# Performance work log

Hardware: AMD Instinct MI355X
Metric: run time of the kernel (lower is better)

Reference implementation:

```python
import jax, jax.numpy as jnp
import numpy as np

B, S, HID = 2, 2048, 2048
H = 16
HD = HID // H            # 128
HD2 = HD // 2            # 64 (rope dim per head)
LAT = HID // 8           # 256 latent dim
BASE = 10000.0


def _rotary_table(seq_len):
    # inv_freq over rope dim HD2
    inv_freq = 1.0 / (BASE ** (jnp.arange(0, HD2, 2, dtype=jnp.float32) / HD2))  # [HD2//2]
    pos = jnp.arange(seq_len, dtype=jnp.float32)
    sincos = pos[:, None] * inv_freq[None, :]                 # [S, HD2//2]
    return jnp.concatenate([jnp.sin(sincos), jnp.cos(sincos)], axis=-1)  # [S, HD2]


def _apply_rope(x, emb):
    # x: [B, S, H, HD2]; emb: [S, HD2]
    half = HD2 // 2
    x1, x2 = x[..., :half], x[..., half:]
    sin = emb[None, :, None, :half]
    cos = emb[None, :, None, half:]
    return jnp.concatenate([x1 * cos - x2 * sin, x1 * sin + x2 * cos], axis=-1)


def setup_inputs() -> dict:
    key = jax.random.key(0)
    ks = jax.random.split(key, 9)
    s = 0.02
    return {
        "hidden_states": jax.random.normal(ks[0], (B, S, HID), jnp.float32),
        "w_kv_d": jax.random.normal(ks[1], (HID, LAT), jnp.float32) * s,
        "w_q_d": jax.random.normal(ks[2], (HID, LAT), jnp.float32) * s,
        "w_k_u": jax.random.normal(ks[3], (LAT, H * HD2), jnp.float32) * s,
        "w_q_u": jax.random.normal(ks[4], (LAT, H * HD2), jnp.float32) * s,
        "w_v_u": jax.random.normal(ks[5], (LAT, H * HD), jnp.float32) * s,
        "w_rope_k": jax.random.normal(ks[6], (HID, HID // 2), jnp.float32) * s,
        "w_rope_q": jax.random.normal(ks[7], (LAT, HID // 2), jnp.float32) * s,
        "w_o": jax.random.normal(ks[8], (HID, HID), jnp.float32) * s,
    }


def reference(hidden_states, w_kv_d, w_q_d, w_k_u, w_q_u, w_v_u, w_rope_k, w_rope_q, w_o):
    b, s, _ = hidden_states.shape
    kv_d = hidden_states @ w_kv_d            # [B,S,LAT]
    q_d = hidden_states @ w_q_d              # [B,S,LAT]
    k_p = (kv_d @ w_k_u).reshape(b, s, H, HD2)
    q_p = (q_d @ w_q_u).reshape(b, s, H, HD2)
    v = (kv_d @ w_v_u).reshape(b, s, H, HD)
    k_r = (hidden_states @ w_rope_k).reshape(b, s, H, HD2)
    q_r = (q_d @ w_rope_q).reshape(b, s, H, HD2)

    emb = _rotary_table(s)
    k_r = _apply_rope(k_r, emb)
    q_r = _apply_rope(q_r, emb)

    k = jnp.concatenate([k_p, k_r], axis=-1)  # [B,S,H,HD]
    q = jnp.concatenate([q_p, q_r], axis=-1)

    scores = jnp.einsum('bqhd,bkhd->bhqk', q, k) / jnp.sqrt(jnp.float32(HD))
    causal = jnp.tril(jnp.ones((s, s), dtype=bool))
    scores = jnp.where(causal[None, None], scores, jnp.float32(-1e9))
    probs = jax.nn.softmax(scores, axis=-1)
    out = jnp.einsum('bhqk,bkhd->bqhd', probs, v).reshape(b, s, HID)
    return out @ w_o
```

## Files before the change

kernel.cpp:

```cpp
#include <hip/hip_runtime.h>
#include <hip/hip_bf16.h>

#define BB 2
#define SS 2048
#define HID 2048
#define NH 16
#define BS (BB*SS)
#define SCALE 0.088388347648318447f
#define C2LOG 0.12751743f

typedef __bf16 bf16x8 __attribute__((ext_vector_type(8)));
typedef float f32x4 __attribute__((ext_vector_type(4)));
typedef float f32x16 __attribute__((ext_vector_type(16)));
typedef unsigned int uintx2 __attribute__((ext_vector_type(2)));

__device__ __forceinline__ bf16x8 ld_frag(const __hip_bfloat16* p) {
    uint4 u = *reinterpret_cast<const uint4*>(p);
    return __builtin_bit_cast(bf16x8, u);
}
__device__ __forceinline__ void store_c(__hip_bfloat16* C, size_t idx, float v) {
    C[idx] = __float2bfloat16(v);
}
__device__ __forceinline__ void store_c(float* C, size_t idx, float v) {
    C[idx] = v;
}
__device__ __forceinline__ ushort bf_bits(float v) {
    __hip_bfloat16 h = __float2bfloat16(v);
    return *reinterpret_cast<ushort*>(&h);
}

#define GLD16(gp, lp) \
  __builtin_amdgcn_global_load_lds((const __attribute__((address_space(1))) void*)(gp), \
                                   (__attribute__((address_space(3))) void*)(lp), 16, 0, 0)

__global__ __launch_bounds__(256) void convert_kernel(
    const float* __restrict__ src, __hip_bfloat16* __restrict__ dst, int n8)
{
    int i = blockIdx.x * blockDim.x + threadIdx.x;
    if (i >= n8) return;
    float4 a = reinterpret_cast<const float4*>(src)[2 * i];
    float4 b = reinterpret_cast<const float4*>(src)[2 * i + 1];
    ushort u[8] = { bf_bits(a.x), bf_bits(a.y), bf_bits(a.z), bf_bits(a.w),
                    bf_bits(b.x), bf_bits(b.y), bf_bits(b.z), bf_bits(b.w) };
    reinterpret_cast<uint4*>(dst)[i] = *reinterpret_cast<uint4*>(u);
}

__global__ __launch_bounds__(256) void transpose_weights_kernel(
    const float* s0, const float* s1, const float* s2, const float* s3,
    const float* s4, const float* s5, const float* s6, const float* s7,
    __hip_bfloat16* WT1, __hip_bfloat16* WT2, __hip_bfloat16* WT3,
    __hip_bfloat16* WTo)
{
    const float* srcs[8] = { s0, s1, s2, s3, s4, s5, s6, s7 };
    const int Rs[8] = { 2048, 2048, 2048, 256, 256, 256, 256, 2048 };
    const int Cs[8] = { 256, 256, 1024, 1024, 2048, 1024, 1024, 2048 };
    __hip_bfloat16* dsts[8] = {
        WT1, WT1 + (size_t)256 * 2048, WT1 + (size_t)512 * 2048,
        WT2, WT2 + (size_t)1024 * 256,
        WT3, WT3 + (size_t)1024 * 256,
        WTo };
    const int prefix[9] = { 0, 512, 1024, 3072, 3328, 3840, 4096, 4352, 8448 };

    int bid = blockIdx.x;
    int seg = 0;
    #pragma unroll
    for (int i = 0; i < 8; i++) if (bid >= prefix[i + 1]) seg = i + 1;
    int local = bid - prefix[seg];
    int R = Rs[seg], C = Cs[seg];
    int tilesC = C / 32;
    int tr = local / tilesC, tc = local % tilesC;
    int r0 = tr * 32, c0 = tc * 32;
    const float* src = srcs[seg];
    __hip_bfloat16* dst = dsts[seg];

    __shared__ float Ts[32][33];
    int t = threadIdx.x;
    int ty = t >> 5, tx = t & 31;
    #pragma unroll
    for (int k = 0; k < 4; k++) {
        int r = ty + k * 8;
        Ts[r][tx] = src[(size_t)(r0 + r) * C + c0 + tx];
    }
    __syncthreads();
    #pragma unroll
    for (int k = 0; k < 4; k++) {
        int r = ty + k * 8;
        dst[(size_t)(c0 + r) * R + r0 + tx] = __float2bfloat16(Ts[tx][r]);
    }
}

template <typename TC>
__global__ __launch_bounds__(256) void gemm_bt_kernel(
    const __hip_bfloat16* __restrict__ A, int lda,
    const __hip_bfloat16* __restrict__ Bt,
    TC* __restrict__ C0, int ldc0, int sp0, int off0, float cm0,
    TC* __restrict__ C1, int ldc1, int sp1, int off1, float cm1,
    int splitN, int K)
{
    __shared__ alignas(16) __hip_bfloat16 As[128 * 32];
    __shared__ alignas(16) __hip_bfloat16 Bs[128 * 32];

    const int bn = blockIdx.x * 128;
    const int bm = blockIdx.y * 128;
    const int t = threadIdx.x;
    const int w = t >> 6;
    const int lane = t & 63;
    const int l15 = lane & 15;
    const int quad = lane >> 4;
    const int wm = (w & 1) * 64;
    const int wn = (w >> 1) * 64;

    const int srow = lane >> 2;
    const int skcol = (lane & 3) * 8;

    f32x4 acc[4][4] = {};

    for (int k0 = 0; k0 < K; k0 += 32) {
        __syncthreads();
        #pragma unroll
        for (int i = 0; i < 2; i++) {
            int r = w * 32 + i * 16 + srow;
            GLD16(A + (size_t)(bm + r) * lda + k0 + skcol, &As[r * 32 + skcol]);
            GLD16(Bt + (size_t)(bn + r) * K + k0 + skcol, &Bs[r * 32 + skcol]);
        }
        __syncthreads();

        bf16x8 af[4], bf[4];
        #pragma unroll
        for (int mt = 0; mt < 4; mt++)
            af[mt] = ld_frag(&As[(wm + mt * 16 + l15) * 32 + quad * 8]);
        #pragma unroll
        for (int nt = 0; nt < 4; nt++)
            bf[nt] = ld_frag(&Bs[(wn + nt * 16 + l15) * 32 + quad * 8]);
        #pragma unroll
        for (int mt = 0; mt < 4; mt++)
            #pragma unroll
            for (int nt = 0; nt < 4; nt++)
                acc[mt][nt] = __builtin_amdgcn_mfma_f32_16x16x32_bf16(
                    af[mt], bf[nt], acc[mt][nt], 0, 0, 0);
    }

    #pragma unroll
    for (int nt = 0; nt < 4; nt++) {
        int col = bn + wn + nt * 16 + l15;
        TC* Cp; int c, ld, s64, off; float cm;
        if (col < splitN) { Cp = C0; c = col; ld = ldc0; s64 = sp0; off = off0; cm = cm0; }
        else { Cp = C1; c = col - splitN; ld = ldc1; s64 = sp1; off = off1; cm = cm1; }
        if (s64 == 2) {
            #pragma unroll
            for (int mt = 0; mt < 4; mt++) {
                int row0 = bm + wm + mt * 16 + quad * 4;
                #pragma unroll
                for (int r = 0; r < 4; r++)
                    store_c(Cp, (size_t)c * 4096 + row0 + r, acc[mt][nt][r] * cm);
            }
        } else {
            int oc = s64 ? ((c >> 6) * 128 + (c & 63) + off) : c;
            #pragma unroll
            for (int mt = 0; mt < 4; mt++) {
                #pragma unroll
                for (int r = 0; r < 4; r++) {
                    int row = bm + wm + mt * 16 + quad * 4 + r;
                    store_c(Cp, (size_t)row * ld + oc, acc[mt][nt][r] * cm);
                }
            }
        }
    }
}

__global__ __launch_bounds__(256) void rope_kernel(
    __hip_bfloat16* __restrict__ Kb, __hip_bfloat16* __restrict__ Qb)
{
    int idx = blockIdx.x * blockDim.x + threadIdx.x;
    if (idx >= BS * NH * 32) return;
    int i = idx & 31;
    int h = (idx >> 5) & 15;
    int row = idx >> 9;
    int s = row & (SS - 1);

    float inv = exp2f(-(float)i * 0.4152410118609203f);
    float ang = (float)s * inv;
    float sn = sinf(ang), cs = cosf(ang);

    size_t obase = (size_t)row * 2048 + h * 128 + 64 + i;
    {
        float x1 = __bfloat162float(Kb[obase]);
        float x2 = __bfloat162float(Kb[obase + 32]);
        Kb[obase]      = __float2bfloat16(x1 * cs - x2 * sn);
        Kb[obase + 32] = __float2bfloat16(x1 * sn + x2 * cs);
    }
    {
        float x1 = __bfloat162float(Qb[obase]);
        float x2 = __bfloat162float(Qb[obase + 32]);
        Qb[obase]      = __float2bfloat16(x1 * cs - x2 * sn);
        Qb[obase + 32] = __float2bfloat16(x1 * sn + x2 * cs);
    }
}

__global__ __launch_bounds__(512) void flash_attn_kernel(
    const __hip_bfloat16* __restrict__ Q,
    const __hip_bfloat16* __restrict__ Kb,
    const __hip_bfloat16* __restrict__ Vt,
    __hip_bfloat16* __restrict__ O)
{
    __shared__ alignas(16) __hip_bfloat16 Ktd[2 * 4 * 64 * 32];
    __shared__ alignas(16) __hip_bfloat16 Vs[2 * 128 * 32];

    const int p = blockIdx.x;
    const int h = blockIdx.y;
    const int b = blockIdx.z;
    const int t = threadIdx.x;
    const int w = t >> 6;
    const int lane = t & 63;
    const int l31 = lane & 31;
    const int hi = lane >> 5;
    const int swl = (l31 >> 1) & 3;

    const int qt = (w < 4) ? (15 - p) : p;
    const int wq = w & 3;
    const int q = qt * 128 + wq * 32 + l31;
    const int my_nt = 2 * qt + 2;
    const int nbig = 2 * (15 - p) + 2;

    const __hip_bfloat16* Kbase = Kb + (size_t)(b * SS) * 2048 + h * 128;
    const __hip_bfloat16* Vtb = Vt + (size_t)(h * 128) * 4096 + b * SS;

    bf16x8 qf[8];
    {
        const __hip_bfloat16* qrow = Q + (size_t)(b * SS + q) * 2048 + h * 128;
        #pragma unroll
        for (int s = 0; s < 8; s++)
            qf[s] = ld_frag(qrow + s * 16 + hi * 8);
    }

    const int Lr = lane >> 2;
    const int Lc = (lane & 3) ^ ((lane >> 3) & 3);

    float m_i = -INFINITY;
    float l_i = 0.0f;
    f32x16 acc[4] = {};

    const int kds = w >> 1, khalf = w & 1;
    const int vkvh = w >> 2, vdq = w & 3;

    #pragma unroll
    for (int i = 0; i < 2; i++)
        GLD16(Kbase + (size_t)(khalf * 32 + i * 16 + Lr) * 2048 + kds * 32 + Lc * 8,
              &Ktd[kds * 2048 + khalf * 1024 + i * 512 + lane * 8]);
    asm volatile("" :: "v"(qf[0]), "v"(qf[1]), "v"(qf[2]), "v"(qf[3]),
                       "v"(qf[4]), "v"(qf[5]), "v"(qf[6]), "v"(qf[7]));

    for (int kt = 0; kt < nbig; kt++) {
        const int kvb = kt * 64;
        const int par = kt & 1;
        const bool active = (kt < my_nt);

        __builtin_amdgcn_s_barrier();
        asm volatile("" ::: "memory");

        #pragma unroll
        for (int i = 0; i < 2; i++)
            GLD16(Vtb + (size_t)(vdq * 32 + i * 16 + Lr) * 4096
                      + kvb + vkvh * 32 + Lc * 8,
                  &Vs[vkvh * 4096 + vdq * 1024 + i * 512 + lane * 8]);
        {
            const int kvb1 = ((kt + 1 < nbig) ? kt + 1 : nbig - 1) * 64;
            __hip_bfloat16* kdst = &Ktd[((kt + 1) & 1) * 8192 + kds * 2048 + khalf * 1024];
            #pragma unroll
            for (int i = 0; i < 2; i++)
                GLD16(Kbase + (size_t)(kvb1 + khalf * 32 + i * 16 + Lr) * 2048
                          + kds * 32 + Lc * 8,
                      kdst + i * 512 + lane * 8);
        }
        asm volatile("s_waitcnt vmcnt(4)" ::: "memory");
        __builtin_amdgcn_s_barrier();
        asm volatile("" ::: "memory");

        uint4 af[4];
        if (active) {
            const __hip_bfloat16* kb_base = &Ktd[par * 8192];
            f32x16 st[2] = {};
            #pragma unroll
            for (int s = 0; s < 8; s++)
                #pragma unroll
                for (int kb = 0; kb < 2; kb++) {
                    bf16x8 kf = ld_frag(kb_base + (s >> 1) * 2048 + (kb * 32 + l31) * 32
                                        + ((2 * (s & 1) + hi) ^ swl) * 8);
                    st[kb] = __builtin_amdgcn_mfma_f32_32x32x16_bf16(
                        kf, qf[s], st[kb], 0, 0, 0);
                }

            const int thr = q - kvb - 4 * hi;
            float tmx = -INFINITY;
            #pragma unroll
            for (int kb = 0; kb < 2; kb++)
                #pragma unroll
                for (int g = 0; g < 4; g++)
                    #pragma unroll
                    for (int r = 0; r < 4; r++) {
                        const int e = g * 4 + r;
                        float v = (kb * 32 + 8 * g + r <= thr) ? st[kb][e] : -INFINITY;
                        st[kb][e] = v;
                        tmx = fmaxf(tmx, v);
                    }
            tmx = fmaxf(tmx, __shfl_xor(tmx, 32));
            const float m2x = tmx * C2LOG;

            const bool nosc = __all(m2x <= m_i + 8.0f);
            const float mnew = nosc ? m_i : fmaxf(m_i, m2x);
            float rs = 0.0f;
            #pragma unroll
            for (int kb = 0; kb < 2; kb++)
                #pragma unroll
                for (int e = 0; e < 16; e++) {
                    float pv = exp2f(fmaf(st[kb][e], C2LOG, -mnew));
                    st[kb][e] = pv;
                    rs += pv;
                }
            rs += __shfl_xor(rs, 32);
            if (!nosc) {
                const float alpha = exp2f(m_i - mnew);
                m_i = mnew;
                l_i *= alpha;
                #pragma unroll
                for (int dt = 0; dt < 4; dt++)
                    #pragma unroll
                    for (int e = 0; e < 16; e++)
                        acc[dt][e] *= alpha;
            }
            l_i += rs;

            #pragma unroll
            for (int kb = 0; kb < 2; kb++) {
                unsigned int pk[4][2];
                #pragma unroll
                for (int g = 0; g < 4; g++)
                    #pragma unroll
                    for (int i = 0; i < 2; i++) {
                        float2 fp = make_float2(st[kb][g * 4 + 2 * i],
                                                st[kb][g * 4 + 2 * i + 1]);
                        __hip_bfloat162 h2 = __float22bfloat162_rn(fp);
                        pk[g][i] = *reinterpret_cast<unsigned int*>(&h2);
                    }
                #pragma unroll
                for (int sl = 0; sl < 2; sl++) {
                    uintx2 r0 = __builtin_amdgcn_permlane32_swap(
                        pk[2 * sl][0], pk[2 * sl + 1][0], false, false);
                    uintx2 r1 = __builtin_amdgcn_permlane32_swap(
                        pk[2 * sl][1], pk[2 * sl + 1][1], false, false);
                    af[kb * 2 + sl] = make_uint4(r0[0], r1[0], r0[1], r1[1]);
                }
            }
        }

        asm volatile("s_waitcnt vmcnt(2)" ::: "memory");
        __builtin_amdgcn_s_barrier();
        asm volatile("" ::: "memory");

        if (active) {
            #pragma unroll
            for (int s = 0; s < 4; s++) {
                bf16x8 pf = __builtin_bit_cast(bf16x8, af[s]);
                #pragma unroll
                for (int dt = 0; dt < 4; dt++) {
                    bf16x8 vf = ld_frag(&Vs[(s >> 1) * 4096 + (dt * 32 + l31) * 32
                                            + ((2 * (s & 1) + hi) ^ swl) * 8]);
                    acc[dt] = __builtin_amdgcn_mfma_f32_32x32x16_bf16(
                        vf, pf, acc[dt], 0, 0, 0);
                }
            }
        }
    }

    const float inv_l = 1.0f / l_i;
    __hip_bfloat16* orow = O + (size_t)(b * SS + q) * 2048 + h * 128;
    #pragma unroll
    for (int dt = 0; dt < 4; dt++)
        #pragma unroll
        for (int g = 0; g < 4; g++) {
            ushort u[4];
            #pragma unroll
            for (int r = 0; r < 4; r++)
                u[r] = bf_bits(acc[dt][g * 4 + r] * inv_l);
            *reinterpret_cast<uint2*>(orow + dt * 32 + 8 * g + 4 * hi) =
                *reinterpret_cast<uint2*>(u);
        }
}

extern "C" void kernel_launch(void* const* d_in, const int* in_sizes, int n_in,
                              void* d_out, int out_size, void* d_ws, size_t ws_size,
                              hipStream_t stream)
{
    const float* hs       = (const float*)d_in[0];
    const float* w_kv_d   = (const float*)d_in[1];
    const float* w_q_d    = (const float*)d_in[2];
    const float* w_k_u    = (const float*)d_in[3];
    const float* w_q_u    = (const float*)d_in[4];
    const float* w_v_u    = (const float*)d_in[5];
    const float* w_rope_k = (const float*)d_in[6];
    const float* w_rope_q = (const float*)d_in[7];
    const float* w_o      = (const float*)d_in[8];
    float* out = (float*)d_out;

    char* p = (char*)d_ws;
    auto alloc = [&](size_t nelem) {
        __hip_bfloat16* r = (__hip_bfloat16*)p;
        p += nelem * sizeof(__hip_bfloat16);
        return r;
    };
    __hip_bfloat16* hsb  = alloc((size_t)BS * HID);
    __hip_bfloat16* qkvd = alloc((size_t)BS * 512);
    __hip_bfloat16* WT1  = alloc((size_t)1536 * 2048);
    __hip_bfloat16* WT2  = alloc((size_t)3072 * 256);
    __hip_bfloat16* WT3  = alloc((size_t)2048 * 256);
    __hip_bfloat16* WTo  = alloc((size_t)2048 * 2048);
    __hip_bfloat16* Kbuf = alloc((size_t)BS * HID);
    __hip_bfloat16* Qbuf = alloc((size_t)BS * HID);
    __hip_bfloat16* Vtb  = alloc((size_t)HID * BS);
    __hip_bfloat16* attn = hsb;

    dim3 blk(256);

    convert_kernel<<<dim3((BS * HID / 8 + 255) / 256), blk, 0, stream>>>(
        hs, hsb, BS * HID / 8);
    transpose_weights_kernel<<<dim3(8448), blk, 0, stream>>>(
        w_kv_d, w_q_d, w_rope_k, w_k_u, w_v_u, w_q_u, w_rope_q, w_o,
        WT1, WT2, WT3, WTo);

    gemm_bt_kernel<__hip_bfloat16><<<dim3(1536 / 128, BS / 128), blk, 0, stream>>>(
        hsb, 2048, WT1,
        qkvd, 512, 0, 0, 1.0f,
        Kbuf, 2048, 1, 64, 1.0f,
        512, 2048);
    gemm_bt_kernel<__hip_bfloat16><<<dim3(3072 / 128, BS / 128), blk, 0, stream>>>(
        qkvd, 512, WT2,
        Kbuf, 2048, 1, 0, 1.0f,
        Vtb, 0, 2, 0, 1.0f,
        1024, 256);
    gemm_bt_kernel<__hip_bfloat16><<<dim3(2048 / 128, BS / 128), blk, 0, stream>>>(
        qkvd + 256, 512, WT3,
        Qbuf, 2048, 1, 0, 1.0f,
        Qbuf, 2048, 1, 64, 1.0f,
        1024, 256);
    rope_kernel<<<dim3((BS * NH * 32 + 255) / 256), blk, 0, stream>>>(Kbuf, Qbuf);
    flash_attn_kernel<<<dim3(8, NH, BB), dim3(512), 0, stream>>>(
        Qbuf, Kbuf, Vtb, attn);
    gemm_bt_kernel<float><<<dim3(2048 / 128, BS / 128), blk, 0, stream>>>(
        attn, 2048, WTo,
        out, 2048, 0, 0, 1.0f,
        out, 2048, 0, 0, 1.0f,
        2048, 2048);
}
```

Baseline: 360.2 us.

## Double-buffer V tiles with K prefetch and drop mid-iteration barrier

V tiles are now double-buffered in shared memory and prefetched one iteration ahead together with K, so the second per-iteration barrier and its vmcnt wait go away. Causal masking is skipped for tiles that lie fully below the diagonal, and each wave's tile count is trimmed so the upper half of the query block skips the last partially masked tile. MFMA sections are wrapped in s_setprio to favour matrix issue across waves. Shared-memory use grows, which may lower occupancy.

```diff
diff --git a/kernel.cpp b/kernel.cpp
--- a/kernel.cpp
+++ b/kernel.cpp
@@ -204,7 +204,7 @@
     __hip_bfloat16* __restrict__ O)
 {
     __shared__ alignas(16) __hip_bfloat16 Ktd[2 * 4 * 64 * 32];
-    __shared__ alignas(16) __hip_bfloat16 Vs[2 * 128 * 32];
+    __shared__ alignas(16) __hip_bfloat16 Vsd[2 * 2 * 128 * 32];
 
     const int p = blockIdx.x;
     const int h = blockIdx.y;
@@ -218,8 +218,9 @@
 
     const int qt = (w < 4) ? (15 - p) : p;
     const int wq = w & 3;
-    const int q = qt * 128 + wq * 32 + l31;
-    const int my_nt = 2 * qt + 2;
+    const int qwb = qt * 128 + wq * 32;
+    const int q = qwb + l31;
+    const int my_nt = 2 * qt + 1 + (wq >> 1);
     const int nbig = 2 * (15 - p) + 2;
 
     const __hip_bfloat16* Kbase = Kb + (size_t)(b * SS) * 2048 + h * 128;
@@ -235,18 +236,21 @@
 
     const int Lr = lane >> 2;
     const int Lc = (lane & 3) ^ ((lane >> 3) & 3);
+    const int kds = w >> 1, khalf = w & 1;
+    const int vkvh = w >> 2, vdq = w & 3;
 
     float m_i = -INFINITY;
     float l_i = 0.0f;
     f32x16 acc[4] = {};
 
-    const int kds = w >> 1, khalf = w & 1;
-    const int vkvh = w >> 2, vdq = w & 3;
-
     #pragma unroll
     for (int i = 0; i < 2; i++)
         GLD16(Kbase + (size_t)(khalf * 32 + i * 16 + Lr) * 2048 + kds * 32 + Lc * 8,
               &Ktd[kds * 2048 + khalf * 1024 + i * 512 + lane * 8]);
+    #pragma unroll
+    for (int i = 0; i < 2; i++)
+        GLD16(Vtb + (size_t)(vdq * 32 + i * 16 + Lr) * 4096 + vkvh * 32 + Lc * 8,
+              &Vsd[vkvh * 4096 + vdq * 1024 + i * 512 + lane * 8]);
     asm volatile("" :: "v"(qf[0]), "v"(qf[1]), "v"(qf[2]), "v"(qf[3]),
                        "v"(qf[4]), "v"(qf[5]), "v"(qf[6]), "v"(qf[7]));
 
@@ -258,28 +262,30 @@
         __builtin_amdgcn_s_barrier();
         asm volatile("" ::: "memory");
 
-        #pragma unroll
-        for (int i = 0; i < 2; i++)
-            GLD16(Vtb + (size_t)(vdq * 32 + i * 16 + Lr) * 4096
-                      + kvb + vkvh * 32 + Lc * 8,
-                  &Vs[vkvh * 4096 + vdq * 1024 + i * 512 + lane * 8]);
         {
-            const int kvb1 = ((kt + 1 < nbig) ? kt + 1 : nbig - 1) * 64;
-            __hip_bfloat16* kdst = &Ktd[((kt + 1) & 1) * 8192 + kds * 2048 + khalf * 1024];
+            const int kvb1 = ((kt + 1 < nbig) ? kt + 1 : kt) * 64;
+            const int pn = (par ^ 1) * 8192;
             #pragma unroll
             for (int i = 0; i < 2; i++)
                 GLD16(Kbase + (size_t)(kvb1 + khalf * 32 + i * 16 + Lr) * 2048
                           + kds * 32 + Lc * 8,
-                      kdst + i * 512 + lane * 8);
+                      &Ktd[pn + kds * 2048 + khalf * 1024 + i * 512 + lane * 8]);
+            #pragma unroll
+            for (int i = 0; i < 2; i++)
+                GLD16(Vtb + (size_t)(vdq * 32 + i * 16 + Lr) * 4096
+                          + kvb1 + vkvh * 32 + Lc * 8,
+                      &Vsd[pn + vkvh * 4096 + vdq * 1024 + i * 512 + lane * 8]);
         }
         asm volatile("s_waitcnt vmcnt(4)" ::: "memory");
         __builtin_amdgcn_s_barrier();
         asm volatile("" ::: "memory");
 
-        uint4 af[4];
         if (active) {
             const __hip_bfloat16* kb_base = &Ktd[par * 8192];
+            const __hip_bfloat16* vb_base = &Vsd[par * 8192];
+
             f32x16 st[2] = {};
+            __builtin_amdgcn_s_setprio(1);
             #pragma unroll
             for (int s = 0; s < 8; s++)
                 #pragma unroll
@@ -289,20 +295,29 @@
                     st[kb] = __builtin_amdgcn_mfma_f32_32x32x16_bf16(
                         kf, qf[s], st[kb], 0, 0, 0);
                 }
-
-            const int thr = q - kvb - 4 * hi;
+            __builtin_amdgcn_s_setprio(0);
+
             float tmx = -INFINITY;
-            #pragma unroll
-            for (int kb = 0; kb < 2; kb++)
-                #pragma unroll
-                for (int g = 0; g < 4; g++)
+            if (kvb + 63 > qwb) {
+                const int thr = q - kvb - 4 * hi;
+                #pragma unroll
+                for (int kb = 0; kb < 2; kb++)
                     #pragma unroll
-                    for (int r = 0; r < 4; r++) {
-                        const int e = g * 4 + r;
-                        float v = (kb * 32 + 8 * g + r <= thr) ? st[kb][e] : -INFINITY;
-                        st[kb][e] = v;
-                        tmx = fmaxf(tmx, v);
-                    }
+                    for (int g = 0; g < 4; g++)
+                        #pragma unroll
+                        for (int r = 0; r < 4; r++) {
+                            const int e = g * 4 + r;
+                            float v = (kb * 32 + 8 * g + r <= thr) ? st[kb][e] : -INFINITY;
+                            st[kb][e] = v;
+                            tmx = fmaxf(tmx, v);
+                        }
+            } else {
+                #pragma unroll
+                for (int kb = 0; kb < 2; kb++)
+                    #pragma unroll
+                    for (int e = 0; e < 16; e++)
+                        tmx = fmaxf(tmx, st[kb][e]);
+            }
             tmx = fmaxf(tmx, __shfl_xor(tmx, 32));
             const float m2x = tmx * C2LOG;
 
@@ -330,6 +345,7 @@
             }
             l_i += rs;
 
+            uint4 af[4];
             #pragma unroll
             for (int kb = 0; kb < 2; kb++) {
                 unsigned int pk[4][2];
@@ -351,24 +367,20 @@
                     af[kb * 2 + sl] = make_uint4(r0[0], r1[0], r0[1], r1[1]);
                 }
             }
-        }
-
-        asm volatile("s_waitcnt vmcnt(2)" ::: "memory");
-        __builtin_amdgcn_s_barrier();
-        asm volatile("" ::: "memory");
-
-        if (active) {
+
+            __builtin_amdgcn_s_setprio(1);
             #pragma unroll
             for (int s = 0; s < 4; s++) {
                 bf16x8 pf = __builtin_bit_cast(bf16x8, af[s]);
                 #pragma unroll
                 for (int dt = 0; dt < 4; dt++) {
-                    bf16x8 vf = ld_frag(&Vs[(s >> 1) * 4096 + (dt * 32 + l31) * 32
-                                            + ((2 * (s & 1) + hi) ^ swl) * 8]);
+                    bf16x8 vf = ld_frag(vb_base + (s >> 1) * 4096 + (dt * 32 + l31) * 32
+                                        + ((2 * (s & 1) + hi) ^ swl) * 8);
                     acc[dt] = __builtin_amdgcn_mfma_f32_32x32x16_bf16(
                         vf, pf, acc[dt], 0, 0, 0);
                 }
             }
+            __builtin_amdgcn_s_setprio(0);
         }
     }
 
```

Result: faster. 347.6 us (-3.5%).
